# Kernel optimization log

Hardware: AMD Instinct MI355X
Metric: run time of the kernel (lower is better)

## Reference

```python
import jax, jax.numpy as jnp
import numpy as np

N_NODES = 50000
N_EDGES = 800000
D = 64          # node_in_feats == out_feats
N_STEPS = 3


def setup_inputs() -> dict:
    key = jax.random.key(0)
    ks = jax.random.split(key, 9)
    s = 1.0 / np.sqrt(D)
    return {
        "node_in": jax.random.normal(ks[0], (N_NODES, D), jnp.float32),
        # edge-type-0 linear (DGL GatedGraphConv self.linears[0])
        "W": jax.random.uniform(ks[1], (D, D), jnp.float32, -s, s),
        "b": jax.random.uniform(ks[2], (D,), jnp.float32, -s, s),
        # GRUCell params (torch layout: rows = [r, z, n] blocks)
        "Wih": jax.random.uniform(ks[3], (3 * D, D), jnp.float32, -s, s),
        "Whh": jax.random.uniform(ks[4], (3 * D, D), jnp.float32, -s, s),
        "bih": jax.random.uniform(ks[5], (3 * D,), jnp.float32, -s, s),
        "bhh": jax.random.uniform(ks[6], (3 * D,), jnp.float32, -s, s),
        "src": jax.random.randint(ks[7], (N_EDGES,), 0, N_NODES, jnp.int32),
        "dst": jax.random.randint(ks[8], (N_EDGES,), 0, N_NODES, jnp.int32),
    }


def _gru_cell(x, h, Wih, Whh, bih, bhh):
    gi = x @ Wih.T + bih   # [N, 3D]
    gh = h @ Whh.T + bhh   # [N, 3D]
    i_r, i_z, i_n = jnp.split(gi, 3, axis=-1)
    h_r, h_z, h_n = jnp.split(gh, 3, axis=-1)
    r = jax.nn.sigmoid(i_r + h_r)
    z = jax.nn.sigmoid(i_z + h_z)
    n = jnp.tanh(i_n + r * h_n)
    return (1.0 - z) * n + z * h


def reference(node_in, W, b, Wih, Whh, bih, bhh, src, dst):
    # DGL GatedGraphConv, n_steps=3, n_etypes=1. node_in_feats == out_feats,
    # so no zero-padding needed. The wrapper's tanh/dropout result is
    # discarded (h is overwritten by the second conv1 call), so the module
    # output is exactly one GatedGraphConv forward.
    h = node_in
    for _ in range(N_STEPS):
        wh = h @ W.T + b                                   # per-node transform; edge msg = wh[src]
        msg = wh[src]                                      # [E, D] gather
        a = jax.ops.segment_sum(msg, dst, num_segments=N_NODES)  # scatter-sum aggregation
        h = _gru_cell(a, h, Wih, Whh, bih, bhh)
    return h
```

## Files before the change

kernel.cpp:

```cpp
#include <hip/hip_runtime.h>

#define D 64
#define EXS 388
#define SGS 72
#define CHUNK 4096
#define PTH 512
#define MAXB 4096

typedef __bf16 bf16x8 __attribute__((ext_vector_type(8)));
typedef float f32x4 __attribute__((ext_vector_type(4)));

union U16 { uint4 u; bf16x8 b; };

__device__ __forceinline__ unsigned short f2bf(float f) {
    unsigned u = __float_as_uint(f);
    u += 0x7fff + ((u >> 16) & 1);
    return (unsigned short)(u >> 16);
}
__device__ __forceinline__ float bf2f(unsigned short s) {
    return __uint_as_float(((unsigned)s) << 16);
}


__global__ __launch_bounds__(PTH) void setup_kernel(const float* __restrict__ in,
                                                    unsigned short* __restrict__ hb0,
                                                    unsigned short* __restrict__ hb1,
                                                    const float* __restrict__ W,
                                                    const float* __restrict__ Wih,
                                                    const float* __restrict__ Whh,
                                                    const float* __restrict__ b,
                                                    unsigned short* __restrict__ Bpack,
                                                    float* __restrict__ cvec,
                                                    const int* __restrict__ src,
                                                    const int* __restrict__ dst,
                                                    int* __restrict__ gcursor,
                                                    unsigned* __restrict__ pairs,
                                                    int n4, int nCvt, int N, int NBUK, int E) {
    __shared__ unsigned pl[CHUNK];
    __shared__ unsigned short bk[CHUNK];
    __shared__ int hist[512];
    __shared__ int wpart[8];
    __shared__ int goff[512];

    if ((int)blockIdx.x < nCvt) {
        int i = blockIdx.x * PTH + threadIdx.x;
        if (i < n4) {
            float4 v = ((const float4*)in)[i];
            ushort4 o;
            o.x = f2bf(v.x); o.y = f2bf(v.y); o.z = f2bf(v.z); o.w = f2bf(v.w);
            ((ushort4*)hb0)[i] = o;
        }
        if (blockIdx.x == 0 && threadIdx.x < 16) {
            ((ushort4*)(hb0 + (size_t)N * D))[threadIdx.x] = (ushort4){0, 0, 0, 0};
            ((ushort4*)(hb1 + (size_t)N * D))[threadIdx.x] = (ushort4){0, 0, 0, 0};
        }
        return;
    }
    int blk = blockIdx.x - nCvt;
    if (blk < 24) {
        if (threadIdx.x >= 128) return;
        int g = blk >> 2, t = blk & 3;
        int ks = threadIdx.x >> 6, lane = threadIdx.x & 63;
        int col = (g % 3) * 64 + t * 16 + (lane & 15);
        int kbase = ks * 32 + ((lane >> 4) & 3) * 8;
        size_t base = ((size_t)(blk * 2 + ks) * 64 + lane) * 8;
#pragma unroll
        for (int j = 0; j < 8; ++j) {
            int k = kbase + j;
            float v;
            if (g < 3) {
                v = 0.f;
#pragma unroll
                for (int m = 0; m < D; ++m) v += Wih[col * D + m] * W[m * D + k];
            } else {
                v = Whh[col * D + k];
            }
            Bpack[base + j] = f2bf(v);
        }
        if (g < 3 && ks == 0 && ((lane >> 4) & 3) == 0) {
            float acc = 0.f;
#pragma unroll
            for (int k = 0; k < D; ++k) acc += Wih[col * D + k] * b[k];
            cvec[col] = acc;
        }
        return;
    }
    {
        int g = blk - 24;
        int t = threadIdx.x;
        int beg = g * CHUNK;
        int end = min(beg + CHUNK, E);
        int m = end - beg;
        hist[t] = 0;
        __syncthreads();
        for (int i = t; i < m; i += PTH)
            atomicAdd(&hist[dst[beg + i] >> 7], 1);
        __syncthreads();
        int own = hist[t];
        int lane6 = t & 63, wv6 = t >> 6;
        int v = own;
#pragma unroll
        for (int off = 1; off < 64; off <<= 1) {
            int nv = __shfl_up(v, off, 64);
            if (lane6 >= off) v += nv;
        }
        if (lane6 == 63) wpart[wv6] = v;
        __syncthreads();
        int basep = 0;
#pragma unroll
        for (int i = 0; i < 8; ++i) basep += (i < wv6) ? wpart[i] : 0;
        int excl = v + basep - own;
        hist[t] = excl;
        if (t < NBUK) {
            int gbase = own ? atomicAdd(&gcursor[t], own) : 0;
            goff[t] = t * MAXB + gbase - excl;
        }
        __syncthreads();
        for (int i = t; i < m; i += PTH) {
            int d = dst[beg + i];
            int s = src[beg + i];
            int bb = d >> 7;
            int pos = atomicAdd(&hist[bb], 1);
            pl[pos] = ((unsigned)s << 7) | (unsigned)(d & 127);
            bk[pos] = (unsigned short)bb;
        }
        __syncthreads();
        for (int i = t; i < m; i += PTH)
            pairs[goff[bk[i]] + i] = pl[i];
    }
}


__global__ __launch_bounds__(512) void bucket_sort_kernel(const unsigned* __restrict__ pairs,
                                                          const int* __restrict__ gcnt,
                                                          int* __restrict__ srcs_sorted,
                                                          int* __restrict__ row_beg,
                                                          int* __restrict__ row_end,
                                                          int NBUK, int N) {
    __shared__ unsigned pl[MAXB];
    __shared__ int srcl[MAXB];
    __shared__ int cnt[128];
    __shared__ int wpart[2];
    __shared__ int cur2[128];
    int b = blockIdx.x;
    int t = threadIdx.x;
    int beg = b * MAXB;
    int m = gcnt[b];
    if (m > MAXB) m = MAXB;
    if (t < 128) cnt[t] = 0;
    __syncthreads();
    for (int i = t; i < m; i += 512) {
        unsigned p = pairs[beg + i];
        pl[i] = p;
        atomicAdd(&cnt[p & 127], 1);
    }
    __syncthreads();
    int vt = (t < 128) ? cnt[t] : 0;
    int lane6 = t & 63, wv6 = t >> 6;
    int v = vt;
#pragma unroll
    for (int off = 1; off < 64; off <<= 1) {
        int nv = __shfl_up(v, off, 64);
        if (lane6 >= off) v += nv;
    }
    if (t < 128 && lane6 == 63) wpart[wv6] = v;
    __syncthreads();
    if (t < 128) {
        int basep = (wv6 == 1) ? wpart[0] : 0;
        int excl = v + basep - vt;
        int gid = b * 128 + t;
        if (gid < N) {
            row_beg[gid] = beg + excl;
            row_end[gid] = beg + excl + vt;
        }
        cur2[t] = excl;
    }
    __syncthreads();
    for (int i = t; i < m; i += 512) {
        unsigned p = pl[i];
        int r = atomicAdd(&cur2[p & 127], 1);
        srcl[r] = (int)(p >> 7);
    }
    __syncthreads();
    for (int i = t; i < m; i += 512) srcs_sorted[beg + i] = srcl[i];
}


__global__ __launch_bounds__(512) void fused2_kernel(const unsigned short* __restrict__ hb_in,
                                                     unsigned short* __restrict__ hb_out,
                                                     float* __restrict__ Fout, int writeF32,
                                                     const unsigned short* __restrict__ Bpack,
                                                     const float* __restrict__ cvec,
                                                     const float* __restrict__ bih,
                                                     const float* __restrict__ bhh,
                                                     const int* __restrict__ row_beg,
                                                     const int* __restrict__ row_end,
                                                     const int* __restrict__ srcs,
                                                     int N) {
    __shared__ unsigned short sg[16 * SGS];
    __shared__ float ex[16 * EXS];
    int tid = threadIdx.x;
    int g = tid >> 6;
    int lane = tid & 63;
    int base = blockIdx.x * 16;

    {
        int es = lane >> 3;
        int fo = lane & 7;
        int nlA = g, nlB = g + 8;
        int nodeA = base + nlA, nodeB = base + nlB;
        int begA = 0, endA = 0, begB = 0, endB = 0;
        if (nodeA < N) { begA = row_beg[nodeA]; endA = row_end[nodeA]; }
        if (nodeB < N) { begB = row_beg[nodeB]; endB = row_end[nodeB]; }

        int sA[4], sB[4];
#pragma unroll
        for (int j = 0; j < 4; ++j) {
            int eA = begA + 8 * j + es;
            int eB = begB + 8 * j + es;
            sA[j] = (eA < endA) ? srcs[eA] : N;
            sB[j] = (eB < endB) ? srcs[eB] : N;
        }
        uint4 dA[4], dB[4];
#pragma unroll
        for (int j = 0; j < 4; ++j) dA[j] = *(const uint4*)(hb_in + (size_t)sA[j] * D + fo * 8);
#pragma unroll
        for (int j = 0; j < 4; ++j) dB[j] = *(const uint4*)(hb_in + (size_t)sB[j] * D + fo * 8);

        float accA[8], accB[8];
#pragma unroll
        for (int j = 0; j < 8; ++j) { accA[j] = 0.f; accB[j] = 0.f; }
#pragma unroll
        for (int j = 0; j < 4; ++j) {
            unsigned ua[4] = {dA[j].x, dA[j].y, dA[j].z, dA[j].w};
            unsigned ub[4] = {dB[j].x, dB[j].y, dB[j].z, dB[j].w};
#pragma unroll
            for (int k = 0; k < 4; ++k) {
                accA[2 * k]     += bf2f((unsigned short)(ua[k] & 0xffff));
                accA[2 * k + 1] += bf2f((unsigned short)(ua[k] >> 16));
                accB[2 * k]     += bf2f((unsigned short)(ub[k] & 0xffff));
                accB[2 * k + 1] += bf2f((unsigned short)(ub[k] >> 16));
            }
        }
        for (int i = begA + 32; i < endA; i += 8) {
            int e = i + es;
            int s = (e < endA) ? srcs[e] : N;
            uint4 dd = *(const uint4*)(hb_in + (size_t)s * D + fo * 8);
            unsigned uu[4] = {dd.x, dd.y, dd.z, dd.w};
#pragma unroll
            for (int k = 0; k < 4; ++k) {
                accA[2 * k]     += bf2f((unsigned short)(uu[k] & 0xffff));
                accA[2 * k + 1] += bf2f((unsigned short)(uu[k] >> 16));
            }
        }
        for (int i = begB + 32; i < endB; i += 8) {
            int e = i + es;
            int s = (e < endB) ? srcs[e] : N;
            uint4 dd = *(const uint4*)(hb_in + (size_t)s * D + fo * 8);
            unsigned uu[4] = {dd.x, dd.y, dd.z, dd.w};
#pragma unroll
            for (int k = 0; k < 4; ++k) {
                accB[2 * k]     += bf2f((unsigned short)(uu[k] & 0xffff));
                accB[2 * k + 1] += bf2f((unsigned short)(uu[k] >> 16));
            }
        }
#pragma unroll
        for (int st = 8; st < 64; st <<= 1)
#pragma unroll
            for (int j = 0; j < 8; ++j) {
                accA[j] += __shfl_xor(accA[j], st, 64);
                accB[j] += __shfl_xor(accB[j], st, 64);
            }
        if (es == 0) {
            uint4 oA, oB;
            oA.x = (unsigned)f2bf(accA[0]) | ((unsigned)f2bf(accA[1]) << 16);
            oA.y = (unsigned)f2bf(accA[2]) | ((unsigned)f2bf(accA[3]) << 16);
            oA.z = (unsigned)f2bf(accA[4]) | ((unsigned)f2bf(accA[5]) << 16);
            oA.w = (unsigned)f2bf(accA[6]) | ((unsigned)f2bf(accA[7]) << 16);
            oB.x = (unsigned)f2bf(accB[0]) | ((unsigned)f2bf(accB[1]) << 16);
            oB.y = (unsigned)f2bf(accB[2]) | ((unsigned)f2bf(accB[3]) << 16);
            oB.z = (unsigned)f2bf(accB[4]) | ((unsigned)f2bf(accB[5]) << 16);
            oB.w = (unsigned)f2bf(accB[6]) | ((unsigned)f2bf(accB[7]) << 16);
            *(uint4*)(sg + nlA * SGS + fo * 8) = oA;
            *(uint4*)(sg + nlB * SGS + fo * 8) = oB;
        }
    }
    __syncthreads();

    if (g < 6) {
        int r16 = lane & 15, quad = lane >> 4;
        bf16x8 bf[4][2];
        const uint4* bp = (const uint4*)Bpack;
#pragma unroll
        for (int t = 0; t < 4; ++t)
#pragma unroll
            for (int ks = 0; ks < 2; ++ks) {
                U16 u; u.u = bp[((g * 4 + t) * 2 + ks) * 64 + lane];
                bf[t][ks] = u.b;
            }
        bf16x8 af[2];
        if (g < 3) {
#pragma unroll
            for (int ks = 0; ks < 2; ++ks) {
                U16 u; u.u = *(const uint4*)(sg + r16 * SGS + ks * 32 + quad * 8);
                af[ks] = u.b;
            }
        } else {
            int row = base + r16;
            if (row >= N) row = N - 1;
#pragma unroll
            for (int ks = 0; ks < 2; ++ks) {
                U16 u; u.u = *(const uint4*)(hb_in + (size_t)row * D + ks * 32 + quad * 8);
                af[ks] = u.b;
            }
        }
        f32x4 acc[4];
#pragma unroll
        for (int t = 0; t < 4; ++t) acc[t] = (f32x4){0.f, 0.f, 0.f, 0.f};
#pragma unroll
        for (int t = 0; t < 4; ++t)
#pragma unroll
            for (int ks = 0; ks < 2; ++ks)
                acc[t] = __builtin_amdgcn_mfma_f32_16x16x32_bf16(af[ks], bf[t][ks], acc[t], 0, 0, 0);
#pragma unroll
        for (int t = 0; t < 4; ++t)
#pragma unroll
            for (int r = 0; r < 4; ++r)
                ex[(quad * 4 + r) * EXS + g * 64 + t * 16 + r16] = acc[t][r];
    }
    __syncthreads();

    for (int idx = tid; idx < 16 * D; idx += 512) {
        int i = idx >> 6, d = idx & 63;
        int node = base + i;
        if (node < N) {
            const float* p = &ex[i * EXS];
            float deg = (float)(row_end[node] - row_beg[node]);
            float ir = p[d] + bih[d] + deg * cvec[d];
            float iz = p[64 + d] + bih[64 + d] + deg * cvec[64 + d];
            float in_ = p[128 + d] + bih[128 + d] + deg * cvec[128 + d];
            float hr = p[192 + d] + bhh[d];
            float hz = p[256 + d] + bhh[64 + d];
            float hn = p[320 + d] + bhh[128 + d];
            float h = bf2f(hb_in[(size_t)node * D + d]);
            float r = 1.f / (1.f + __expf(-(ir + hr)));
            float z = 1.f / (1.f + __expf(-(iz + hz)));
            float nn = tanhf(in_ + r * hn);
            float hnew = (1.f - z) * nn + z * h;
            if (writeF32) Fout[(size_t)node * D + d] = hnew;
            else hb_out[(size_t)node * D + d] = f2bf(hnew);
        }
    }
}

extern "C" void kernel_launch(void* const* d_in, const int* in_sizes, int n_in,
                              void* d_out, int out_size, void* d_ws, size_t ws_size,
                              hipStream_t stream) {
    const float* node_in = (const float*)d_in[0];
    const float* W       = (const float*)d_in[1];
    const float* b       = (const float*)d_in[2];
    const float* Wih     = (const float*)d_in[3];
    const float* Whh     = (const float*)d_in[4];
    const float* bih     = (const float*)d_in[5];
    const float* bhh     = (const float*)d_in[6];
    const int*   src     = (const int*)d_in[7];
    const int*   dst     = (const int*)d_in[8];
    const int N = in_sizes[0] / D;
    const int E = in_sizes[7];
    float* out = (float*)d_out;

    const int G = (E + CHUNK - 1) / CHUNK;
    const int NBUK = (N + 127) >> 7;

    char* ws = (char*)d_ws;
    size_t off = 0;
    auto alloc = [&](size_t bytes) -> void* {
        void* p = ws + off;
        off += (bytes + 255) & ~(size_t)255;
        return p;
    };
    unsigned short* hb0    = (unsigned short*)alloc((size_t)(N + 1) * D * 2);
    unsigned short* hb1    = (unsigned short*)alloc((size_t)(N + 1) * D * 2);
    int*   row_beg         = (int*)alloc((size_t)NBUK * 128 * sizeof(int));
    int*   row_end         = (int*)alloc((size_t)NBUK * 128 * sizeof(int));
    int*   srcs_sorted     = (int*)alloc((size_t)NBUK * MAXB * sizeof(int));
    unsigned* pairs        = (unsigned*)alloc((size_t)NBUK * MAXB * sizeof(unsigned));
    int*   gcursor         = (int*)alloc((size_t)NBUK * sizeof(int));
    unsigned short* Bpack  = (unsigned short*)alloc((size_t)6 * 4 * 2 * 64 * 8 * 2);
    float* cvec            = (float*)alloc((size_t)192 * sizeof(float));

    hipMemsetAsync(gcursor, 0, (size_t)NBUK * sizeof(int), stream);

    const int n4 = N * D / 4;
    const int nCvt = (n4 + PTH - 1) / PTH;
    setup_kernel<<<nCvt + 24 + G, PTH, 0, stream>>>(node_in, hb0, hb1, W, Wih, Whh, b,
                                                    Bpack, cvec, src, dst, gcursor, pairs,
                                                    n4, nCvt, N, NBUK, E);

    bucket_sort_kernel<<<NBUK, 512, 0, stream>>>(pairs, gcursor, srcs_sorted,
                                                 row_beg, row_end, NBUK, N);

    const int grid = (N + 15) / 16;
    fused2_kernel<<<grid, 512, 0, stream>>>(hb0, hb1, out, 0, Bpack, cvec, bih, bhh,
                                            row_beg, row_end, srcs_sorted, N);
    fused2_kernel<<<grid, 512, 0, stream>>>(hb1, hb0, out, 0, Bpack, cvec, bih, bhh,
                                            row_beg, row_end, srcs_sorted, N);
    fused2_kernel<<<grid, 512, 0, stream>>>(hb0, hb1, out, 1, Bpack, cvec, bih, bhh,
                                            row_beg, row_end, srcs_sorted, N);
}
```

Before: 201.7 us.

## Sort nodes by degree within buckets and specialize gather unroll depth

The bucket sort kernel now bins the 128 nodes of each bucket by in-degree and writes a node permutation. The fused GRU kernels then process nodes in that order, so the paired nodes handled by each wavefront have similar degree. The gather step also dispatches to an unroll depth of 1–4 based on the larger degree of the pair. This is meant to cut wasted masked loads and divergence on low-degree nodes. The cost is an extra indirection through nodemap, scattered output writes, and reads of padded node ids, which are handled through the N bound checks.

```diff
diff --git a/kernel.cpp b/kernel.cpp
--- a/kernel.cpp
+++ b/kernel.cpp
@@ -19,6 +19,38 @@
 }
 __device__ __forceinline__ float bf2f(unsigned short s) {
     return __uint_as_float(((unsigned)s) << 16);
+}
+
+__device__ __forceinline__ void addrow(float* acc, uint4 dd) {
+    unsigned uu[4] = {dd.x, dd.y, dd.z, dd.w};
+#pragma unroll
+    for (int k = 0; k < 4; ++k) {
+        acc[2 * k]     += bf2f((unsigned short)(uu[k] & 0xffff));
+        acc[2 * k + 1] += bf2f((unsigned short)(uu[k] >> 16));
+    }
+}
+
+template <int R>
+__device__ __forceinline__ void gatherR(float* accA, float* accB,
+                                        const int* __restrict__ srcs,
+                                        const unsigned short* __restrict__ hb,
+                                        int begA, int endA, int begB, int endB,
+                                        int es, int fo, int N) {
+    int sA[R], sB[R];
+#pragma unroll
+    for (int j = 0; j < R; ++j) {
+        int eA = begA + 8 * j + es;
+        int eB = begB + 8 * j + es;
+        sA[j] = (eA < endA) ? srcs[eA] : N;
+        sB[j] = (eB < endB) ? srcs[eB] : N;
+    }
+    uint4 dA[R], dB[R];
+#pragma unroll
+    for (int j = 0; j < R; ++j) dA[j] = *(const uint4*)(hb + (size_t)sA[j] * D + fo * 8);
+#pragma unroll
+    for (int j = 0; j < R; ++j) dB[j] = *(const uint4*)(hb + (size_t)sB[j] * D + fo * 8);
+#pragma unroll
+    for (int j = 0; j < R; ++j) { addrow(accA, dA[j]); addrow(accB, dB[j]); }
 }
 
 
@@ -136,18 +168,22 @@
                                                           int* __restrict__ srcs_sorted,
                                                           int* __restrict__ row_beg,
                                                           int* __restrict__ row_end,
+                                                          int* __restrict__ nodemap,
                                                           int NBUK, int N) {
     __shared__ unsigned pl[MAXB];
     __shared__ int srcl[MAXB];
     __shared__ int cnt[128];
     __shared__ int wpart[2];
     __shared__ int cur2[128];
+    __shared__ int bins[64];
+    __shared__ int binbase[64];
     int b = blockIdx.x;
     int t = threadIdx.x;
     int beg = b * MAXB;
     int m = gcnt[b];
     if (m > MAXB) m = MAXB;
     if (t < 128) cnt[t] = 0;
+    if (t < 64) bins[t] = 0;
     __syncthreads();
     for (int i = t; i < m; i += 512) {
         unsigned p = pairs[beg + i];
@@ -156,6 +192,8 @@
     }
     __syncthreads();
     int vt = (t < 128) ? cnt[t] : 0;
+    int kbin = min(vt, 63);
+    if (t < 128) atomicAdd(&bins[kbin], 1);
     int lane6 = t & 63, wv6 = t >> 6;
     int v = vt;
 #pragma unroll
@@ -165,6 +203,16 @@
     }
     if (t < 128 && lane6 == 63) wpart[wv6] = v;
     __syncthreads();
+    if (t < 64) {
+        int bv = bins[t];
+        int sv = bv;
+#pragma unroll
+        for (int off = 1; off < 64; off <<= 1) {
+            int nv = __shfl_up(sv, off, 64);
+            if (t >= off) sv += nv;
+        }
+        binbase[t] = sv - bv;
+    }
     if (t < 128) {
         int basep = (wv6 == 1) ? wpart[0] : 0;
         int excl = v + basep - vt;
@@ -176,6 +224,10 @@
         cur2[t] = excl;
     }
     __syncthreads();
+    if (t < 128) {
+        int pos = atomicAdd(&binbase[kbin], 1);
+        nodemap[b * 128 + pos] = b * 128 + t;
+    }
     for (int i = t; i < m; i += 512) {
         unsigned p = pl[i];
         int r = atomicAdd(&cur2[p & 127], 1);
@@ -196,6 +248,7 @@
                                                      const int* __restrict__ row_beg,
                                                      const int* __restrict__ row_end,
                                                      const int* __restrict__ srcs,
+                                                     const int* __restrict__ nodemap,
                                                      int N) {
     __shared__ unsigned short sg[16 * SGS];
     __shared__ float ex[16 * EXS];
@@ -208,62 +261,42 @@
         int es = lane >> 3;
         int fo = lane & 7;
         int nlA = g, nlB = g + 8;
-        int nodeA = base + nlA, nodeB = base + nlB;
+        int nodeA = nodemap[base + nlA], nodeB = nodemap[base + nlB];
         int begA = 0, endA = 0, begB = 0, endB = 0;
         if (nodeA < N) { begA = row_beg[nodeA]; endA = row_end[nodeA]; }
         if (nodeB < N) { begB = row_beg[nodeB]; endB = row_end[nodeB]; }
 
-        int sA[4], sB[4];
-#pragma unroll
-        for (int j = 0; j < 4; ++j) {
-            int eA = begA + 8 * j + es;
-            int eB = begB + 8 * j + es;
-            sA[j] = (eA < endA) ? srcs[eA] : N;
-            sB[j] = (eB < endB) ? srcs[eB] : N;
-        }
-        uint4 dA[4], dB[4];
-#pragma unroll
-        for (int j = 0; j < 4; ++j) dA[j] = *(const uint4*)(hb_in + (size_t)sA[j] * D + fo * 8);
-#pragma unroll
-        for (int j = 0; j < 4; ++j) dB[j] = *(const uint4*)(hb_in + (size_t)sB[j] * D + fo * 8);
-
         float accA[8], accB[8];
 #pragma unroll
         for (int j = 0; j < 8; ++j) { accA[j] = 0.f; accB[j] = 0.f; }
-#pragma unroll
-        for (int j = 0; j < 4; ++j) {
-            unsigned ua[4] = {dA[j].x, dA[j].y, dA[j].z, dA[j].w};
-            unsigned ub[4] = {dB[j].x, dB[j].y, dB[j].z, dB[j].w};
-#pragma unroll
-            for (int k = 0; k < 4; ++k) {
-                accA[2 * k]     += bf2f((unsigned short)(ua[k] & 0xffff));
-                accA[2 * k + 1] += bf2f((unsigned short)(ua[k] >> 16));
-                accB[2 * k]     += bf2f((unsigned short)(ub[k] & 0xffff));
-                accB[2 * k + 1] += bf2f((unsigned short)(ub[k] >> 16));
-            }
-        }
-        for (int i = begA + 32; i < endA; i += 8) {
-            int e = i + es;
-            int s = (e < endA) ? srcs[e] : N;
-            uint4 dd = *(const uint4*)(hb_in + (size_t)s * D + fo * 8);
-            unsigned uu[4] = {dd.x, dd.y, dd.z, dd.w};
-#pragma unroll
-            for (int k = 0; k < 4; ++k) {
-                accA[2 * k]     += bf2f((unsigned short)(uu[k] & 0xffff));
-                accA[2 * k + 1] += bf2f((unsigned short)(uu[k] >> 16));
-            }
-        }
-        for (int i = begB + 32; i < endB; i += 8) {
-            int e = i + es;
-            int s = (e < endB) ? srcs[e] : N;
-            uint4 dd = *(const uint4*)(hb_in + (size_t)s * D + fo * 8);
-            unsigned uu[4] = {dd.x, dd.y, dd.z, dd.w};
-#pragma unroll
-            for (int k = 0; k < 4; ++k) {
-                accB[2 * k]     += bf2f((unsigned short)(uu[k] & 0xffff));
-                accB[2 * k + 1] += bf2f((unsigned short)(uu[k] >> 16));
-            }
-        }
+
+        int dmax = max(endA - begA, endB - begB);
+        if (dmax > 0) {
+            if (dmax <= 8)
+                gatherR<1>(accA, accB, srcs, hb_in, begA, endA, begB, endB, es, fo, N);
+            else if (dmax <= 16)
+                gatherR<2>(accA, accB, srcs, hb_in, begA, endA, begB, endB, es, fo, N);
+            else if (dmax <= 24)
+                gatherR<3>(accA, accB, srcs, hb_in, begA, endA, begB, endB, es, fo, N);
+            else {
+                gatherR<4>(accA, accB, srcs, hb_in, begA, endA, begB, endB, es, fo, N);
+                if (dmax > 32) {
+                    for (int i = begA + 32; i < endA; i += 8) {
+                        int e = i + es;
+                        int s = (e < endA) ? srcs[e] : N;
+                        uint4 dd = *(const uint4*)(hb_in + (size_t)s * D + fo * 8);
+                        addrow(accA, dd);
+                    }
+                    for (int i = begB + 32; i < endB; i += 8) {
+                        int e = i + es;
+                        int s = (e < endB) ? srcs[e] : N;
+                        uint4 dd = *(const uint4*)(hb_in + (size_t)s * D + fo * 8);
+                        addrow(accB, dd);
+                    }
+                }
+            }
+        }
+
 #pragma unroll
         for (int st = 8; st < 64; st <<= 1)
 #pragma unroll
@@ -306,7 +339,7 @@
                 af[ks] = u.b;
             }
         } else {
-            int row = base + r16;
+            int row = nodemap[base + r16];
             if (row >= N) row = N - 1;
 #pragma unroll
             for (int ks = 0; ks < 2; ++ks) {
@@ -332,7 +365,7 @@
 
     for (int idx = tid; idx < 16 * D; idx += 512) {
         int i = idx >> 6, d = idx & 63;
-        int node = base + i;
+        int node = nodemap[base + i];
         if (node < N) {
             const float* p = &ex[i * EXS];
             float deg = (float)(row_end[node] - row_beg[node]);
@@ -383,6 +416,7 @@
     unsigned short* hb1    = (unsigned short*)alloc((size_t)(N + 1) * D * 2);
     int*   row_beg         = (int*)alloc((size_t)NBUK * 128 * sizeof(int));
     int*   row_end         = (int*)alloc((size_t)NBUK * 128 * sizeof(int));
+    int*   nodemap         = (int*)alloc((size_t)NBUK * 128 * sizeof(int));
     int*   srcs_sorted     = (int*)alloc((size_t)NBUK * MAXB * sizeof(int));
     unsigned* pairs        = (unsigned*)alloc((size_t)NBUK * MAXB * sizeof(unsigned));
     int*   gcursor         = (int*)alloc((size_t)NBUK * sizeof(int));
@@ -398,13 +432,13 @@
                                                     n4, nCvt, N, NBUK, E);
 
     bucket_sort_kernel<<<NBUK, 512, 0, stream>>>(pairs, gcursor, srcs_sorted,
-                                                 row_beg, row_end, NBUK, N);
-
-    const int grid = (N + 15) / 16;
-    fused2_kernel<<<grid, 512, 0, stream>>>(hb0, hb1, out, 0, Bpack, cvec, bih, bhh,
-                                            row_beg, row_end, srcs_sorted, N);
-    fused2_kernel<<<grid, 512, 0, stream>>>(hb1, hb0, out, 0, Bpack, cvec, bih, bhh,
-                                            row_beg, row_end, srcs_sorted, N);
-    fused2_kernel<<<grid, 512, 0, stream>>>(hb0, hb1, out, 1, Bpack, cvec, bih, bhh,
-                                            row_beg, row_end, srcs_sorted, N);
-}
+                                                 row_beg, row_end, nodemap, NBUK, N);
+
+    const int gridF = NBUK * 8;
+    fused2_kernel<<<gridF, 512, 0, stream>>>(hb0, hb1, out, 0, Bpack, cvec, bih, bhh,
+                                             row_beg, row_end, srcs_sorted, nodemap, N);
+    fused2_kernel<<<gridF, 512, 0, stream>>>(hb1, hb0, out, 0, Bpack, cvec, bih, bhh,
+                                             row_beg, row_end, srcs_sorted, nodemap, N);
+    fused2_kernel<<<gridF, 512, 0, stream>>>(hb0, hb1, out, 1, Bpack, cvec, bih, bhh,
+                                             row_beg, row_end, srcs_sorted, nodemap, N);
+}
```

Result: slower. 226.8 us (+12.4%).
